# Kernel tuning notes

Hardware: AMD Instinct MI355X
Metric: run time of the kernel (lower is better)

The kernel has to match this reference:

```python
import jax, jax.numpy as jnp
import numpy as np

N_NODES = 50000
DEG = 16            # fixed average degree -> nnz = N_NODES * DEG
NNZ = N_NODES * DEG
IN_FEATS = 256
OUT_FEATS = 128


def setup_inputs() -> dict:
    key = jax.random.key(0)
    k1, k2, k3, k4, k5, k6, k7 = jax.random.split(key, 7)
    # CSR adjacency: regular DEG edges per row (row_ptr strictly valid)
    row_ptr_s = (jnp.arange(N_NODES + 1, dtype=jnp.int32) * DEG)
    col_idx_s = jax.random.randint(k1, (NNZ,), 0, N_NODES, dtype=jnp.int32)
    edge_val_csr_s = jax.random.uniform(k2, (NNZ,), dtype=jnp.float32)
    # CSC copy (used only by the original CUDA backward kernel; plausible dummies)
    col_ptr_s = (jnp.arange(N_NODES + 1, dtype=jnp.int32) * DEG)
    row_idx_s = jax.random.randint(k3, (NNZ,), 0, N_NODES, dtype=jnp.int32)
    edge_val_csc_s = jax.random.uniform(k4, (NNZ,), dtype=jnp.float32)
    in_feat = jax.random.normal(k5, (N_NODES, IN_FEATS), dtype=jnp.float32)
    # Parameters: xavier-uniform W, zero bias
    limit = float(np.sqrt(6.0 / (IN_FEATS + OUT_FEATS)))
    W = jax.random.uniform(k6, (IN_FEATS, OUT_FEATS), dtype=jnp.float32,
                           minval=-limit, maxval=limit)
    bias = jnp.zeros((OUT_FEATS,), dtype=jnp.float32)
    return {
        "nnz": NNZ,
        "row_ptr_s": row_ptr_s, "col_idx_s": col_idx_s, "edge_val_csr_s": edge_val_csr_s,
        "p_csr": 1, "q_csr": 1,
        "col_ptr_s": col_ptr_s, "row_idx_s": row_idx_s, "edge_val_csc_s": edge_val_csc_s,
        "p_csc": 1, "q_csc": 1,
        "in_feat": in_feat, "W": W, "bias": bias,
    }


def _csr_spmm(row_ptr, col_idx, edge_val, h):
    """out[i] = sum_{e in row i} edge_val[e] * h[col_idx[e]]  (A @ h, A in CSR)."""
    n = row_ptr.shape[0] - 1
    nnz = col_idx.shape[0]
    # map each edge to its destination row via the row pointer
    row_id = jnp.searchsorted(row_ptr, jnp.arange(nnz, dtype=row_ptr.dtype), side="right") - 1
    msg = h[col_idx] * edge_val[:, None]          # [nnz, out_feats]
    return jax.ops.segment_sum(msg, row_id, num_segments=n)


def reference(nnz, row_ptr_s, col_idx_s, edge_val_csr_s, p_csr, q_csr,
              col_ptr_s, row_idx_s, edge_val_csc_s, p_csc, q_csc,
              in_feat, W, bias):
    h = in_feat @ W                                # [N, out_feats]
    rst = _csr_spmm(row_ptr_s, col_idx_s, edge_val_csr_s, h)
    return jax.nn.relu(rst + bias)
```

## Files before the change

### kernel.cpp

```cpp
#include <hip/hip_runtime.h>
#include <hip/hip_bf16.h>

#define IN_F 256
#define OUT_F 128
#define BM 32
#define GEMM_THREADS 512
#define GEMM_BLOCKS 512

typedef __bf16 bf16x8 __attribute__((ext_vector_type(8)));
typedef float  f32x4  __attribute__((ext_vector_type(4)));
typedef int    i32x4  __attribute__((ext_vector_type(4)));

__global__ __launch_bounds__(GEMM_THREADS)
void gemm_xw_kernel(const float* __restrict__ X, const float* __restrict__ W,
                    __bf16* __restrict__ H, int n, int ntiles)
{
    __shared__ __bf16 xs[2][BM * IN_F];

    const int tid  = threadIdx.x;
    const int lane = tid & 63;
    const int wid  = tid >> 6;
    const int wm   = wid >> 2;
    const int wn   = wid & 3;

    const int srow = tid >> 5;
    const int sk   = (tid & 31) * 8;

    int tile = blockIdx.x;
    if (tile < ntiles) {
        const int r0 = tile * BM;
        float4 a0 = make_float4(0,0,0,0), a1 = a0, b0 = a0, b1 = a0;
        const int gr0 = r0 + srow, gr1 = r0 + srow + 16;
        if (gr0 < n) {
            a0 = *(const float4*)(X + (size_t)gr0 * IN_F + sk);
            a1 = *(const float4*)(X + (size_t)gr0 * IN_F + sk + 4);
        }
        if (gr1 < n) {
            b0 = *(const float4*)(X + (size_t)gr1 * IN_F + sk);
            b1 = *(const float4*)(X + (size_t)gr1 * IN_F + sk + 4);
        }
        bf16x8 v0, v1;
        v0[0]=(__bf16)a0.x; v0[1]=(__bf16)a0.y; v0[2]=(__bf16)a0.z; v0[3]=(__bf16)a0.w;
        v0[4]=(__bf16)a1.x; v0[5]=(__bf16)a1.y; v0[6]=(__bf16)a1.z; v0[7]=(__bf16)a1.w;
        v1[0]=(__bf16)b0.x; v1[1]=(__bf16)b0.y; v1[2]=(__bf16)b0.z; v1[3]=(__bf16)b0.w;
        v1[4]=(__bf16)b1.x; v1[5]=(__bf16)b1.y; v1[6]=(__bf16)b1.z; v1[7]=(__bf16)b1.w;
        *(bf16x8*)&xs[0][(srow * IN_F + sk) ^ ((srow & 7) << 3)] = v0;
        *(bf16x8*)&xs[0][((srow + 16) * IN_F + sk) ^ (((srow + 16) & 7) << 3)] = v1;
    }

    bf16x8 bfrag[8][2];
    {
        const int nbase = wn * 32 + (lane & 15);
        const int kbase = (lane >> 4) * 8;
        #pragma unroll
        for (int kk = 0; kk < 8; ++kk) {
            #pragma unroll
            for (int nf = 0; nf < 2; ++nf) {
                #pragma unroll
                for (int j = 0; j < 8; ++j)
                    bfrag[kk][nf][j] =
                        (__bf16)W[(size_t)(kk * 32 + kbase + j) * OUT_F + nbase + nf * 16];
            }
        }
    }
    __syncthreads();

    int cur = 0;
    for (; tile < ntiles; tile += gridDim.x) {
        const int nxt = tile + (int)gridDim.x;
        const bool has_next = nxt < ntiles;

        float4 a0 = make_float4(0,0,0,0), a1 = a0, b0 = a0, b1 = a0;
        if (has_next) {
            const int r0 = nxt * BM;
            const int gr0 = r0 + srow, gr1 = r0 + srow + 16;
            if (gr0 < n) {
                a0 = *(const float4*)(X + (size_t)gr0 * IN_F + sk);
                a1 = *(const float4*)(X + (size_t)gr0 * IN_F + sk + 4);
            }
            if (gr1 < n) {
                b0 = *(const float4*)(X + (size_t)gr1 * IN_F + sk);
                b1 = *(const float4*)(X + (size_t)gr1 * IN_F + sk + 4);
            }
        }

        f32x4 acc0 = (f32x4)0.f, acc1 = (f32x4)0.f;
        {
            const int arow  = wm * 16 + (lane & 15);
            const int akoff = (lane >> 4) * 8;
            #pragma unroll
            for (int kk = 0; kk < 8; ++kk) {
                const int sidx = (arow * IN_F + kk * 32 + akoff) ^ ((arow & 7) << 3);
                const bf16x8 a = *(const bf16x8*)&xs[cur][sidx];
                acc0 = __builtin_amdgcn_mfma_f32_16x16x32_bf16(a, bfrag[kk][0], acc0, 0, 0, 0);
                acc1 = __builtin_amdgcn_mfma_f32_16x16x32_bf16(a, bfrag[kk][1], acc1, 0, 0, 0);
            }
        }

        {
            const int crow0 = tile * BM + wm * 16 + (lane >> 4) * 4;
            const int ccol0 = wn * 32 + (lane & 15);
            #pragma unroll
            for (int j = 0; j < 4; ++j) {
                const int row = crow0 + j;
                if (row < n) {
                    H[(size_t)row * OUT_F + ccol0]      = (__bf16)acc0[j];
                    H[(size_t)row * OUT_F + ccol0 + 16] = (__bf16)acc1[j];
                }
            }
        }

        if (has_next) {
            bf16x8 v0, v1;
            v0[0]=(__bf16)a0.x; v0[1]=(__bf16)a0.y; v0[2]=(__bf16)a0.z; v0[3]=(__bf16)a0.w;
            v0[4]=(__bf16)a1.x; v0[5]=(__bf16)a1.y; v0[6]=(__bf16)a1.z; v0[7]=(__bf16)a1.w;
            v1[0]=(__bf16)b0.x; v1[1]=(__bf16)b0.y; v1[2]=(__bf16)b0.z; v1[3]=(__bf16)b0.w;
            v1[4]=(__bf16)b1.x; v1[5]=(__bf16)b1.y; v1[6]=(__bf16)b1.z; v1[7]=(__bf16)b1.w;
            const int nb = cur ^ 1;
            *(bf16x8*)&xs[nb][(srow * IN_F + sk) ^ ((srow & 7) << 3)] = v0;
            *(bf16x8*)&xs[nb][((srow + 16) * IN_F + sk) ^ (((srow + 16) & 7) << 3)] = v1;
        }
        __syncthreads();
        cur ^= 1;
    }
}

__global__ __launch_bounds__(256, 4)
void spmm_bias_relu_kernel(const int* __restrict__ row_ptr,
                           const int* __restrict__ col_idx,
                           const float* __restrict__ val,
                           const __bf16* __restrict__ H,
                           const float* __restrict__ bias,
                           float* __restrict__ out, int n)
{
    const int row = blockIdx.x * 16 + (threadIdx.x >> 4);
    const int c8  = (threadIdx.x & 15) * 8;
    if (row >= n) return;

    const int s = row_ptr[row];
    const int e = row_ptr[row + 1];

    const f32x4 b0 = *(const f32x4*)(bias + c8);
    const f32x4 b1 = *(const f32x4*)(bias + c8 + 4);

    float acc[8];
    #pragma unroll
    for (int j = 0; j < 8; ++j) acc[j] = 0.f;

    if (e - s == 16 && (s & 3) == 0) {
        i32x4 ci[4];
        f32x4 vi[4];
        #pragma unroll
        for (int i = 0; i < 4; ++i) {
            ci[i] = __builtin_nontemporal_load((const i32x4*)(col_idx + s) + i);
            vi[i] = __builtin_nontemporal_load((const f32x4*)(val + s) + i);
        }
        bf16x8 hv[16];
        #pragma unroll
        for (int i = 0; i < 16; ++i)
            hv[i] = *(const bf16x8*)(H + (size_t)ci[i >> 2][i & 3] * OUT_F + c8);
        #pragma unroll
        for (int i = 0; i < 16; ++i) {
            const float v = vi[i >> 2][i & 3];
            #pragma unroll
            for (int j = 0; j < 8; ++j)
                acc[j] = fmaf(v, (float)hv[i][j], acc[j]);
        }
    } else {
        for (int ee = s; ee < e; ++ee) {
            const int   col = col_idx[ee];
            const float v   = val[ee];
            const bf16x8 hv = *(const bf16x8*)(H + (size_t)col * OUT_F + c8);
            #pragma unroll
            for (int j = 0; j < 8; ++j)
                acc[j] = fmaf(v, (float)hv[j], acc[j]);
        }
    }

    f32x4 o0 = { fmaxf(acc[0] + b0[0], 0.f), fmaxf(acc[1] + b0[1], 0.f),
                 fmaxf(acc[2] + b0[2], 0.f), fmaxf(acc[3] + b0[3], 0.f) };
    f32x4 o1 = { fmaxf(acc[4] + b1[0], 0.f), fmaxf(acc[5] + b1[1], 0.f),
                 fmaxf(acc[6] + b1[2], 0.f), fmaxf(acc[7] + b1[3], 0.f) };
    __builtin_nontemporal_store(o0, (f32x4*)(out + (size_t)row * OUT_F + c8));
    __builtin_nontemporal_store(o1, (f32x4*)(out + (size_t)row * OUT_F + c8 + 4));
}

extern "C" void kernel_launch(void* const* d_in, const int* in_sizes, int n_in,
                              void* d_out, int out_size, void* d_ws, size_t ws_size,
                              hipStream_t stream)
{
    const int*   row_ptr = (const int*)  d_in[1];
    const int*   col_idx = (const int*)  d_in[2];
    const float* edgeval = (const float*)d_in[3];
    const float* in_feat = (const float*)d_in[11];
    const float* W       = (const float*)d_in[12];
    const float* bias    = (const float*)d_in[13];

    const int n = in_sizes[11] / IN_F;

    __bf16* H = (__bf16*)d_ws;

    const int ntiles = (n + BM - 1) / BM;
    const int gemm_blocks = ntiles < GEMM_BLOCKS ? ntiles : GEMM_BLOCKS;
    gemm_xw_kernel<<<gemm_blocks, GEMM_THREADS, 0, stream>>>(in_feat, W, H, n, ntiles);

    const int spmm_blocks = (n + 15) / 16;
    spmm_bias_relu_kernel<<<spmm_blocks, 256, 0, stream>>>(
        row_ptr, col_idx, edgeval, H, bias, (float*)d_out, n);
}
```

Measured before the change: 51.04 us.

## Partition GEMM rows into contiguous per-block chunks instead of strided tiles

The X@W kernel now gives each block a contiguous range of 98 rows and walks it in 32-row sub-tiles, replacing a grid-stride loop over tiles with 512 blocks. This yields about 511 blocks, each covering 4 sub-tiles with the last one partial, to spread work evenly over the CUs. It also makes each block's reads contiguous in memory. The cost is that a partial final sub-tile wastes MFMA work in every block, and W fragments are still reloaded per block.

```diff
diff --git a/kernel.cpp b/kernel.cpp
--- a/kernel.cpp
+++ b/kernel.cpp
@@ -4,8 +4,8 @@
 #define IN_F 256
 #define OUT_F 128
 #define BM 32
+#define ROWS_PER_BLOCK 98
 #define GEMM_THREADS 512
-#define GEMM_BLOCKS 512
 
 typedef __bf16 bf16x8 __attribute__((ext_vector_type(8)));
 typedef float  f32x4  __attribute__((ext_vector_type(4)));
@@ -13,7 +13,7 @@
 
 __global__ __launch_bounds__(GEMM_THREADS)
 void gemm_xw_kernel(const float* __restrict__ X, const float* __restrict__ W,
-                    __bf16* __restrict__ H, int n, int ntiles)
+                    __bf16* __restrict__ H, int n)
 {
     __shared__ __bf16 xs[2][BM * IN_F];
 
@@ -23,19 +23,21 @@
     const int wm   = wid >> 2;
     const int wn   = wid & 3;
 
+    const int lo   = blockIdx.x * ROWS_PER_BLOCK;
+    const int rmax = min(n, lo + ROWS_PER_BLOCK);
+    if (lo >= n) return;
+
     const int srow = tid >> 5;
     const int sk   = (tid & 31) * 8;
 
-    int tile = blockIdx.x;
-    if (tile < ntiles) {
-        const int r0 = tile * BM;
+    {
         float4 a0 = make_float4(0,0,0,0), a1 = a0, b0 = a0, b1 = a0;
-        const int gr0 = r0 + srow, gr1 = r0 + srow + 16;
-        if (gr0 < n) {
+        const int gr0 = lo + srow, gr1 = lo + srow + 16;
+        if (gr0 < rmax) {
             a0 = *(const float4*)(X + (size_t)gr0 * IN_F + sk);
             a1 = *(const float4*)(X + (size_t)gr0 * IN_F + sk + 4);
         }
-        if (gr1 < n) {
+        if (gr1 < rmax) {
             b0 = *(const float4*)(X + (size_t)gr1 * IN_F + sk);
             b1 = *(const float4*)(X + (size_t)gr1 * IN_F + sk + 4);
         }
@@ -66,19 +68,18 @@
     __syncthreads();
 
     int cur = 0;
-    for (; tile < ntiles; tile += gridDim.x) {
-        const int nxt = tile + (int)gridDim.x;
-        const bool has_next = nxt < ntiles;
+    for (int r0 = lo; r0 < rmax; r0 += BM) {
+        const int nr0 = r0 + BM;
+        const bool has_next = nr0 < rmax;
 
         float4 a0 = make_float4(0,0,0,0), a1 = a0, b0 = a0, b1 = a0;
         if (has_next) {
-            const int r0 = nxt * BM;
-            const int gr0 = r0 + srow, gr1 = r0 + srow + 16;
-            if (gr0 < n) {
+            const int gr0 = nr0 + srow, gr1 = nr0 + srow + 16;
+            if (gr0 < rmax) {
                 a0 = *(const float4*)(X + (size_t)gr0 * IN_F + sk);
                 a1 = *(const float4*)(X + (size_t)gr0 * IN_F + sk + 4);
             }
-            if (gr1 < n) {
+            if (gr1 < rmax) {
                 b0 = *(const float4*)(X + (size_t)gr1 * IN_F + sk);
                 b1 = *(const float4*)(X + (size_t)gr1 * IN_F + sk + 4);
             }
@@ -98,12 +99,12 @@
         }
 
         {
-            const int crow0 = tile * BM + wm * 16 + (lane >> 4) * 4;
+            const int crow0 = r0 + wm * 16 + (lane >> 4) * 4;
             const int ccol0 = wn * 32 + (lane & 15);
             #pragma unroll
             for (int j = 0; j < 4; ++j) {
                 const int row = crow0 + j;
-                if (row < n) {
+                if (row < rmax) {
                     H[(size_t)row * OUT_F + ccol0]      = (__bf16)acc0[j];
                     H[(size_t)row * OUT_F + ccol0 + 16] = (__bf16)acc1[j];
                 }
@@ -200,9 +201,8 @@
 
     __bf16* H = (__bf16*)d_ws;
 
-    const int ntiles = (n + BM - 1) / BM;
-    const int gemm_blocks = ntiles < GEMM_BLOCKS ? ntiles : GEMM_BLOCKS;
-    gemm_xw_kernel<<<gemm_blocks, GEMM_THREADS, 0, stream>>>(in_feat, W, H, n, ntiles);
+    const int gemm_blocks = (n + ROWS_PER_BLOCK - 1) / ROWS_PER_BLOCK;
+    gemm_xw_kernel<<<gemm_blocks, GEMM_THREADS, 0, stream>>>(in_feat, W, H, n);
 
     const int spmm_blocks = (n + 15) / 16;
     spmm_bias_relu_kernel<<<spmm_blocks, 256, 0, stream>>>(
```

After: 52.02 us. About the same (+1.9%).
